# Performance work log

Hardware: AMD Instinct MI355X
Metric: run time of the kernel (lower is better)

## Reference

```python
import jax, jax.numpy as jnp
import numpy as np

B, N, D_IN, D_OUT = 4, 1024, 128, 64
SLOPE = 0.01  # LeakyReLU negative slope


def leaky_relu(x):
    return jnp.where(x >= 0, x, SLOPE * x)


def setup_inputs() -> dict:
    key = jax.random.key(0)
    k_x, k_m, k_w1, k_w2, k_a, k_l = jax.random.split(key, 6)
    x = jax.random.normal(k_x, (B, N, D_IN), dtype=jnp.float32)
    # binary adjacency mask; add self-loops so every row has >=1 neighbor
    mask = jax.random.bernoulli(k_m, 0.05, (B, N, N)).astype(jnp.float32)
    eye = jnp.eye(N, dtype=jnp.float32)[None]
    A_shape = jnp.maximum(mask, eye)
    w1 = jax.random.normal(k_w1, (D_IN, D_OUT), dtype=jnp.float32)
    w2 = jax.random.normal(k_w2, (D_IN, D_OUT), dtype=jnp.float32)
    a = jax.random.normal(k_a, (D_OUT,), dtype=jnp.float32)
    lin_w = jax.random.normal(k_l, (D_OUT, D_IN), dtype=jnp.float32) * (1.0 / np.sqrt(D_IN))
    return {"x": x, "A_shape": A_shape, "w1": w1, "w2": w2, "a": a, "lin_w": lin_w}


def reference(x, A_shape, w1, w2, a, lin_w):
    # x: [B,N,D_in], A_shape: [B,N,N] mask
    x1 = x @ w1            # [B,N,D_out]  (dst features)
    x2 = x @ w2            # [B,N,D_out]  (src features)
    # GATv2 additive score: leakyrelu(x1_i + x2_j) . a -> [B,N,N]
    S = leaky_relu(x1[:, :, None, :] + x2[:, None, :, :])
    S = jnp.einsum('bijd,d->bij', S, a)
    S = jnp.tanh(S / 8.0) * 8.0
    A = jnp.exp(S) * A_shape
    A = A / jnp.sum(A, axis=-1, keepdims=True)
    out = A @ x            # [B,N,D_in] weighted aggregate of raw features
    out = out @ lin_w.T    # [B,N,D_out]
    return leaky_relu(out)
```

## Files before the change

kernel.cpp:

```cpp
#include <hip/hip_runtime.h>
#include <math.h>

#define BB 4
#define NN 1024
#define DIN 128
#define DOUT 64
#define SLOPE 0.01f
#define RST 192


__global__ __launch_bounds__(64, 8) void proj_kernel(
    const float* __restrict__ x, const float* __restrict__ w1,
    const float* __restrict__ w2, const float* __restrict__ lin_w,
    float* __restrict__ x12y) {
  int l = threadIdx.x;
  int row = blockIdx.x;
  __shared__ __align__(16) float xl[DIN];
  reinterpret_cast<float2*>(xl)[l] =
      reinterpret_cast<const float2*>(x + (size_t)row * DIN)[l];
  __syncthreads();
  const float* w1c = w1 + l;
  const float* w2c = w2 + l;
  float a1 = 0.f, a2 = 0.f;
#pragma unroll 8
  for (int k = 0; k < DIN; ++k) {
    float xv = xl[k];
    a1 = fmaf(xv, w1c[k * DOUT], a1);
    a2 = fmaf(xv, w2c[k * DOUT], a2);
  }
  const float4* lw4 = reinterpret_cast<const float4*>(lin_w + (size_t)l * DIN);
  float a3 = 0.f;
#pragma unroll 8
  for (int k4 = 0; k4 < DIN / 4; ++k4) {
    float4 wv = lw4[k4];
    a3 = fmaf(xl[4 * k4 + 0], wv.x, a3);
    a3 = fmaf(xl[4 * k4 + 1], wv.y, a3);
    a3 = fmaf(xl[4 * k4 + 2], wv.z, a3);
    a3 = fmaf(xl[4 * k4 + 3], wv.w, a3);
  }
  size_t o = (size_t)row * RST;
  x12y[o + l] = a1;
  x12y[o + DOUT + l] = a2;
  x12y[o + 2 * DOUT + l] = a3;
}

__device__ __forceinline__ float fast_edge_exp(float sc) {
  float z = sc * 0.125f;
  z = fminf(10.f, fmaxf(-10.f, z));
  float u = __expf(2.f * z);
  float th = (u - 1.f) / (u + 1.f);
  return __expf(8.f * th);
}

__global__ __launch_bounds__(128, 8) void gat_row_kernel(
    const float* __restrict__ A_shape, const float* __restrict__ a_vec,
    const float* __restrict__ x12y, float* __restrict__ out) {
  int bi = blockIdx.x;
  int b = bi >> 10;
  int tid = threadIdx.x;
  int lane = tid & 63;
  int w = tid >> 6;

  __shared__ int eidx[1040];
  __shared__ float evals[1040];
  __shared__ __align__(16) float x1s[DOUT];
  __shared__ __align__(16) float avs[DOUT];
  __shared__ float aggh[2][DOUT];
  __shared__ float wsum[2];
  __shared__ int cnt[2];

  if (tid < DOUT) {
    x1s[tid] = x12y[(size_t)bi * RST + tid];
    avs[tid] = a_vec[tid];
  }

  const float* mask_row = A_shape + (size_t)bi * NN + w * 512;
  float mv[8];
#pragma unroll
  for (int c = 0; c < 8; ++c) mv[c] = mask_row[c * 64 + lane];
  int base = 0;
  int seg = w * 512;
#pragma unroll
  for (int c = 0; c < 8; ++c) {
    bool pred = (mv[c] != 0.f);
    unsigned long long m = __ballot(pred);
    int prefix = __popcll(m & ((1ull << lane) - 1ull));
    if (pred) eidx[seg + base + prefix] = w * 512 + c * 64 + lane;
    base += __popcll(m);
  }
  if (lane == 0) cnt[w] = base;
  __syncthreads();

  int nz0 = cnt[0], nz1 = cnt[1];
  int nzt = nz0 + nz1;
  int nzt16 = (nzt + 15) & ~15;
  if (tid < 16) {
    eidx[512 + nz1 + tid] = bi & (NN - 1);
    evals[512 + nz1 + tid] = 0.f;
  }
  __syncthreads();

  const float* x2b = x12y + (size_t)b * NN * RST + DOUT;
  int l16 = tid & 15;
  int grp = tid >> 4;
  float4 x1v = reinterpret_cast<const float4*>(x1s)[l16];
  float4 avv = reinterpret_cast<const float4*>(avs)[l16];
  float lsum = 0.f;
  for (int s = grp; s < nzt; s += 8) {
    int ps = (s < nz0) ? s : 512 + s - nz0;
    int j = eidx[ps];
    float4 x2v = *reinterpret_cast<const float4*>(
        x2b + (size_t)j * RST + l16 * 4);
    float z, sc = 0.f;
    z = x1v.x + x2v.x; sc = fmaf(z >= 0.f ? z : SLOPE * z, avv.x, sc);
    z = x1v.y + x2v.y; sc = fmaf(z >= 0.f ? z : SLOPE * z, avv.y, sc);
    z = x1v.z + x2v.z; sc = fmaf(z >= 0.f ? z : SLOPE * z, avv.z, sc);
    z = x1v.w + x2v.w; sc = fmaf(z >= 0.f ? z : SLOPE * z, avv.w, sc);
    sc += __shfl_xor(sc, 8, 16);
    sc += __shfl_xor(sc, 4, 16);
    sc += __shfl_xor(sc, 2, 16);
    sc += __shfl_xor(sc, 1, 16);
    if (l16 == 0) {
      float e = fast_edge_exp(sc);
      evals[ps] = e;
      lsum += e;
    }
  }

#pragma unroll
  for (int off = 32; off > 0; off >>= 1) lsum += __shfl_xor(lsum, off, 64);
  if (lane == 0) wsum[w] = lsum;
  __syncthreads();
  float inv = 1.f / (wsum[0] + wsum[1]);

  int d = tid & 63;
  int h = tid >> 6;
  const float* yb = x12y + (size_t)b * NN * RST + 2 * DOUT + d;
  float acc0 = 0.f, acc1 = 0.f;
  for (int s = 0; s < nzt16; s += 16) {
    int j[8];
    float wt[8];
#pragma unroll
    for (int r = 0; r < 8; ++r) {
      int ss = s + h + 2 * r;
      int ps = (ss < nz0) ? ss : 512 + ss - nz0;
      j[r] = eidx[ps];
      wt[r] = evals[ps];
    }
    float yv[8];
#pragma unroll
    for (int r = 0; r < 8; ++r) yv[r] = yb[(size_t)j[r] * RST];
#pragma unroll
    for (int r = 0; r < 8; r += 2) {
      acc0 = fmaf(wt[r], yv[r], acc0);
      acc1 = fmaf(wt[r + 1], yv[r + 1], acc1);
    }
  }
  aggh[h][d] = acc0 + acc1;
  __syncthreads();

  if (tid < DOUT) {
    float oo = (aggh[0][tid] + aggh[1][tid]) * inv;
    oo = oo >= 0.f ? oo : SLOPE * oo;
    out[(size_t)bi * DOUT + tid] = oo;
  }
}

extern "C" void kernel_launch(void* const* d_in, const int* in_sizes, int n_in,
                              void* d_out, int out_size, void* d_ws, size_t ws_size,
                              hipStream_t stream) {
  const float* x = (const float*)d_in[0];
  const float* A_shape = (const float*)d_in[1];
  const float* w1 = (const float*)d_in[2];
  const float* w2 = (const float*)d_in[3];
  const float* a = (const float*)d_in[4];
  const float* lin_w = (const float*)d_in[5];
  float* out = (float*)d_out;
  float* x12y = (float*)d_ws;

  proj_kernel<<<BB * NN, 64, 0, stream>>>(x, w1, w2, lin_w, x12y);
  gat_row_kernel<<<BB * NN, 128, 0, stream>>>(A_shape, a, x12y, out);
}
```

Measured before the change: 111.5 us.

## Tile projection kernel over 16 rows per block with shared transposed lin_w

The projection kernel now handles 16 rows per 256-thread block, and each thread accumulates 4 rows so every weight load is reused four times. lin_w is staged into shared memory transposed (padded to avoid bank conflicts) so the third projection reads coalesced columns instead of strided float4 rows per thread. This cuts weight traffic and launch count for the projection stage. In exchange each block does more shared-memory staging, uses more registers, and the grid has fewer blocks.

```diff
diff --git a/kernel.cpp b/kernel.cpp
--- a/kernel.cpp
+++ b/kernel.cpp
@@ -7,41 +7,58 @@
 #define DOUT 64
 #define SLOPE 0.01f
 #define RST 192
-
-
-__global__ __launch_bounds__(64, 8) void proj_kernel(
+#define R1 16
+
+
+__global__ __launch_bounds__(256, 2) void proj_kernel(
     const float* __restrict__ x, const float* __restrict__ w1,
     const float* __restrict__ w2, const float* __restrict__ lin_w,
     float* __restrict__ x12y) {
-  int l = threadIdx.x;
-  int row = blockIdx.x;
-  __shared__ __align__(16) float xl[DIN];
-  reinterpret_cast<float2*>(xl)[l] =
-      reinterpret_cast<const float2*>(x + (size_t)row * DIN)[l];
-  __syncthreads();
-  const float* w1c = w1 + l;
-  const float* w2c = w2 + l;
-  float a1 = 0.f, a2 = 0.f;
-#pragma unroll 8
+  int tid = threadIdx.x;
+  int d = tid & 63;
+  int g = tid >> 6;
+  __shared__ __align__(16) float xl[R1][DIN];
+  __shared__ float lwT[DIN][DOUT + 1];
+  int row0 = blockIdx.x * R1;
+
+  {
+    const float4* xs = reinterpret_cast<const float4*>(x + (size_t)row0 * DIN);
+    float4* xd = reinterpret_cast<float4*>(&xl[0][0]);
+    xd[tid] = xs[tid];
+    xd[tid + 256] = xs[tid + 256];
+  }
+#pragma unroll
+  for (int i = 0; i < 32; ++i) {
+    int idx = i * 256 + tid;
+    lwT[idx & 127][idx >> 7] = lin_w[idx];
+  }
+  __syncthreads();
+
+  float a1[4] = {0.f, 0.f, 0.f, 0.f};
+  float a2[4] = {0.f, 0.f, 0.f, 0.f};
+  float a3[4] = {0.f, 0.f, 0.f, 0.f};
+  const float* w1c = w1 + d;
+  const float* w2c = w2 + d;
+#pragma unroll 4
   for (int k = 0; k < DIN; ++k) {
-    float xv = xl[k];
-    a1 = fmaf(xv, w1c[k * DOUT], a1);
-    a2 = fmaf(xv, w2c[k * DOUT], a2);
-  }
-  const float4* lw4 = reinterpret_cast<const float4*>(lin_w + (size_t)l * DIN);
-  float a3 = 0.f;
-#pragma unroll 8
-  for (int k4 = 0; k4 < DIN / 4; ++k4) {
-    float4 wv = lw4[k4];
-    a3 = fmaf(xl[4 * k4 + 0], wv.x, a3);
-    a3 = fmaf(xl[4 * k4 + 1], wv.y, a3);
-    a3 = fmaf(xl[4 * k4 + 2], wv.z, a3);
-    a3 = fmaf(xl[4 * k4 + 3], wv.w, a3);
-  }
-  size_t o = (size_t)row * RST;
-  x12y[o + l] = a1;
-  x12y[o + DOUT + l] = a2;
-  x12y[o + 2 * DOUT + l] = a3;
+    float wv1 = w1c[k * DOUT];
+    float wv2 = w2c[k * DOUT];
+    float wv3 = lwT[k][d];
+#pragma unroll
+    for (int r = 0; r < 4; ++r) {
+      float xv = xl[g * 4 + r][k];
+      a1[r] = fmaf(xv, wv1, a1[r]);
+      a2[r] = fmaf(xv, wv2, a2[r]);
+      a3[r] = fmaf(xv, wv3, a3[r]);
+    }
+  }
+#pragma unroll
+  for (int r = 0; r < 4; ++r) {
+    size_t o = (size_t)(row0 + g * 4 + r) * RST;
+    x12y[o + d] = a1[r];
+    x12y[o + DOUT + d] = a2[r];
+    x12y[o + 2 * DOUT + d] = a3[r];
+  }
 }
 
 __device__ __forceinline__ float fast_edge_exp(float sc) {
@@ -178,6 +195,6 @@
   float* out = (float*)d_out;
   float* x12y = (float*)d_ws;
 
-  proj_kernel<<<BB * NN, 64, 0, stream>>>(x, w1, w2, lin_w, x12y);
+  proj_kernel<<<BB * NN / R1, 256, 0, stream>>>(x, w1, w2, lin_w, x12y);
   gat_row_kernel<<<BB * NN, 128, 0, stream>>>(A_shape, a, x12y, out);
 }
```

Measured after the change: 99.84 us. 10.5% less time.
